# Optimization experiments

Measured on AMD Instinct MI355X. Metric: run time of the kernel, lower is better.

Reference implementation:

```python
import jax, jax.numpy as jnp
import numpy as np

D_MODEL = 1536
NUM_HEADS = 16
QUERY_GROUPS = 4
HEAD_DIM = D_MODEL // NUM_HEADS  # 96
HEADS_PER_GROUP = NUM_HEADS // QUERY_GROUPS
THETA = 10000.0


def _grid_positions(grid_t, grid_h, grid_w):
    # [N, 3] lookup table of (t, h, w) coords, N = T*H*W, 'ij' meshgrid order
    t, h, w = jnp.meshgrid(jnp.arange(grid_t), jnp.arange(grid_h), jnp.arange(grid_w), indexing='ij')
    return jnp.stack([t.reshape(-1), h.reshape(-1), w.reshape(-1)], axis=-1)


def _rope3d(x, positions):
    # x: [B, N, H, head_dim]; rotate three contiguous head_dim//3 slices, one per axis
    B, N, H, hd = x.shape
    dpa = hd // 3            # dims per axis
    P = dpa // 2             # rotation pairs per axis
    freqs = 1.0 / (THETA ** (jnp.arange(P, dtype=jnp.float32) * 2.0 / dpa))  # same for t/h/w
    parts = []
    for axis in range(3):
        ang = positions[:, axis].astype(jnp.float32)[:, None] * freqs[None, :]  # [N, P]
        cos = jnp.cos(ang)[None, :, None, :]  # [1, N, 1, P]
        sin = jnp.sin(ang)[None, :, None, :]
        sl = x[..., axis * dpa:(axis + 1) * dpa].reshape(B, N, H, P, 2)
        x0, x1 = sl[..., 0], sl[..., 1]
        rot = jnp.stack([x0 * cos - x1 * sin, x0 * sin + x1 * cos], axis=-1)
        parts.append(rot.reshape(B, N, H, dpa))
    return jnp.concatenate(parts, axis=-1)


def setup_inputs() -> dict:
    key = jax.random.key(0)
    k1, k2, k3 = jax.random.split(key, 3)
    B, GT, GH, GW = 2, 8, 16, 16
    N = GT * GH * GW  # 2048
    x = jax.random.normal(k1, (B, N, D_MODEL), dtype=jnp.float32)
    qkv_out = NUM_HEADS * HEAD_DIM + 2 * QUERY_GROUPS * HEAD_DIM  # 2304
    w_qkv = jax.random.normal(k2, (qkv_out, D_MODEL), dtype=jnp.float32) * 0.02
    w_o = jax.random.normal(k3, (D_MODEL, D_MODEL), dtype=jnp.float32) * 0.02
    return {"x": x, "w_qkv": w_qkv, "w_o": w_o, "grid_t": GT, "grid_h": GH, "grid_w": GW}


def reference(x, w_qkv, w_o, grid_t, grid_h, grid_w):
    B, N, _ = x.shape
    qkv = x @ w_qkv.T  # [B, N, 2304]
    q_dim = NUM_HEADS * HEAD_DIM
    kv_dim = QUERY_GROUPS * HEAD_DIM
    q = qkv[..., :q_dim].reshape(B, N, NUM_HEADS, HEAD_DIM)
    k = qkv[..., q_dim:q_dim + kv_dim].reshape(B, N, QUERY_GROUPS, HEAD_DIM)
    v = qkv[..., q_dim + kv_dim:].reshape(B, N, QUERY_GROUPS, HEAD_DIM)

    pos = _grid_positions(grid_t, grid_h, grid_w)  # [N, 3]
    q = _rope3d(q, pos)
    k = _rope3d(k, pos)

    # GQA: repeat_interleave kv heads up to num_heads
    k = jnp.repeat(k, HEADS_PER_GROUP, axis=2)
    v = jnp.repeat(v, HEADS_PER_GROUP, axis=2)

    scale = 1.0 / jnp.sqrt(jnp.asarray(HEAD_DIM, dtype=x.dtype))
    scores = jnp.einsum('bnhd,bmhd->bhnm', q, k) * scale
    attn = jax.nn.softmax(scores, axis=-1)
    out = jnp.einsum('bhnm,bmhd->bnhd', attn, v).reshape(B, N, D_MODEL)
    return out @ w_o.T
```

## Files before the change

### kernel.cpp

```cpp
#include <hip/hip_runtime.h>
#include <hip/hip_bf16.h>

typedef short bf16x8 __attribute__((ext_vector_type(8)));
typedef float f32x4  __attribute__((ext_vector_type(4)));

#define NH    16
#define NG    4
#define HD    96
#define DM    1536
#define BB    2
#define NSEQ  2048
#define QKVD  2304
#define MROWS (BB * NSEQ)

__device__ __forceinline__ short bf16_bits(float v)
{
    __hip_bfloat16 h = __float2bfloat16(v);
    return *reinterpret_cast<short*>(&h);
}

__device__ __forceinline__ void stage16(short* dst, const float* src)
{
    float f[16];
    *(float4*)(f + 0)  = *(const float4*)(src + 0);
    *(float4*)(f + 4)  = *(const float4*)(src + 4);
    *(float4*)(f + 8)  = *(const float4*)(src + 8);
    *(float4*)(f + 12) = *(const float4*)(src + 12);
    bf16x8 v0, v1;
    #pragma unroll
    for (int j = 0; j < 8; ++j) { v0[j] = bf16_bits(f[j]); v1[j] = bf16_bits(f[8 + j]); }
    *(bf16x8*)dst = v0;
    *(bf16x8*)(dst + 8) = v1;
}
__device__ __forceinline__ void stage16(short* dst, const __hip_bfloat16* src)
{
    *(bf16x8*)dst       = *(const bf16x8*)src;
    *(bf16x8*)(dst + 8) = *(const bf16x8*)(src + 8);
}

__device__ __forceinline__ void store_c(__hip_bfloat16* p, float v)
{
    *p = __float2bfloat16(v);
}
__device__ __forceinline__ void store_c(float* p, float v) { *p = v; }

__device__ __forceinline__ void gload_lds16(const short* g, short* lds)
{
    __builtin_amdgcn_global_load_lds(
        (const __attribute__((address_space(1))) unsigned int*)g,
        (__attribute__((address_space(3))) unsigned int*)lds,
        16, 0, 0);
}

__global__ __launch_bounds__(256) void cvt3_bf16(
    const float* __restrict__ x,  short* __restrict__ xb,
    const float* __restrict__ wq, short* __restrict__ wqb,
    const float* __restrict__ wo, short* __restrict__ wob)
{
    const int i = blockIdx.x * 256 + threadIdx.x;
    const float* s; short* d; int off;
    if (i < 786432)       { s = x;  d = xb;  off = i; }
    else if (i < 1228800) { s = wq; d = wqb; off = i - 786432; }
    else                  { s = wo; d = wob; off = i - 1228800; }
    float f[8];
    *(float4*)(f + 0) = *(const float4*)(s + (size_t)off * 8);
    *(float4*)(f + 4) = *(const float4*)(s + (size_t)off * 8 + 4);
    bf16x8 v;
    #pragma unroll
    for (int j = 0; j < 8; ++j) v[j] = bf16_bits(f[j]);
    *(bf16x8*)(d + (size_t)off * 8) = v;
}

template <typename TC>
__global__ __launch_bounds__(256) void gemm_async(
    const short* __restrict__ A,
    const short* __restrict__ B,
    TC* __restrict__ C,
    int M, int Nc, int K, int lda, int ldb, int nbx)
{
    __shared__ __align__(16) short As[128][32];
    __shared__ __align__(16) short Bs[128][32];

    const int tid  = threadIdx.x;
    const int wave = tid >> 6;
    const int lane = tid & 63;
    const int quad = lane >> 4;
    const int l16  = lane & 15;
    const int wm = (wave >> 1) * 64;
    const int wn = (wave & 1) * 64;

    const int cpx = gridDim.x >> 3;
    const int swz = (blockIdx.x & 7) * cpx + (blockIdx.x >> 3);
    const int bx  = swz % nbx;
    const int by  = swz / nbx;
    const int m0 = by * 128;
    const int n0 = bx * 128;

    const int lrow = lane >> 2;
    const int lcol = (lane & 3) * 8;

    f32x4 acc[4][4] = {};

    for (int k0 = 0; k0 < K; k0 += 32) {
        __syncthreads();
        #pragma unroll
        for (int i = 0; i < 2; ++i) {
            const int j = wave * 2 + i;
            gload_lds16(A + (size_t)(m0 + j * 16 + lrow) * lda + k0 + lcol, &As[j * 16][0]);
            gload_lds16(B + (size_t)(n0 + j * 16 + lrow) * ldb + k0 + lcol, &Bs[j * 16][0]);
        }
        __syncthreads();

        bf16x8 af[4], bfr[4];
        #pragma unroll
        for (int i = 0; i < 4; ++i)
            af[i] = *(const bf16x8*)&As[wm + i * 16 + l16][quad * 8];
        #pragma unroll
        for (int j = 0; j < 4; ++j)
            bfr[j] = *(const bf16x8*)&Bs[wn + j * 16 + l16][quad * 8];
        #pragma unroll
        for (int i = 0; i < 4; ++i)
            #pragma unroll
            for (int j = 0; j < 4; ++j)
                acc[i][j] = __builtin_amdgcn_mfma_f32_16x16x32_bf16(
                    af[i], bfr[j], acc[i][j], 0, 0, 0);
    }

    #pragma unroll
    for (int i = 0; i < 4; ++i)
      #pragma unroll
      for (int j = 0; j < 4; ++j)
        #pragma unroll
        for (int r = 0; r < 4; ++r) {
            const int row = m0 + wm + i * 16 + quad * 4 + r;
            const int col = n0 + wn + j * 16 + l16;
            store_c(C + (size_t)row * Nc + col, acc[i][j][r]);
        }
}

#define KSTR 40

template <typename TA, typename TB, typename TC>
__global__ __launch_bounds__(256) void gemm_tiled(
    const TA* __restrict__ A,
    const TB* __restrict__ B,
    TC* __restrict__ C,
    int M, int Nc, int K, int lda)
{
    __shared__ __align__(16) short As[128][KSTR];
    __shared__ __align__(16) short Bs[128][KSTR];

    const int tid  = threadIdx.x;
    const int wave = tid >> 6;
    const int lane = tid & 63;
    const int quad = lane >> 4;
    const int l16  = lane & 15;
    const int wm = (wave >> 1) * 64;
    const int wn = (wave & 1) * 64;
    const int m0 = blockIdx.y * 128;
    const int n0 = blockIdx.x * 128;

    const int srow  = tid >> 1;
    const int skseg = (tid & 1) << 4;
    const TA* Asrc = A + (size_t)(m0 + srow) * lda + skseg;
    const TB* Bsrc = B + (size_t)(n0 + srow) * K + skseg;

    f32x4 acc[4][4] = {};

    for (int k0 = 0; k0 < K; k0 += 32) {
        __syncthreads();
        stage16(&As[srow][skseg], Asrc + k0);
        stage16(&Bs[srow][skseg], Bsrc + k0);
        __syncthreads();

        bf16x8 af[4], bfr[4];
        #pragma unroll
        for (int i = 0; i < 4; ++i)
            af[i] = *(const bf16x8*)&As[wm + i * 16 + l16][quad * 8];
        #pragma unroll
        for (int j = 0; j < 4; ++j)
            bfr[j] = *(const bf16x8*)&Bs[wn + j * 16 + l16][quad * 8];
        #pragma unroll
        for (int i = 0; i < 4; ++i)
            #pragma unroll
            for (int j = 0; j < 4; ++j)
                acc[i][j] = __builtin_amdgcn_mfma_f32_16x16x32_bf16(
                    af[i], bfr[j], acc[i][j], 0, 0, 0);
    }

    #pragma unroll
    for (int i = 0; i < 4; ++i)
      #pragma unroll
      for (int j = 0; j < 4; ++j)
        #pragma unroll
        for (int r = 0; r < 4; ++r) {
            const int row = m0 + wm + i * 16 + quad * 4 + r;
            const int col = n0 + wn + j * 16 + l16;
            store_c(C + (size_t)row * Nc + col, acc[i][j][r]);
        }
}

__global__ __launch_bounds__(256) void rope_inplace(__hip_bfloat16* qkv)
{
    const int e = blockIdx.x * 256 + threadIdx.x;
    if (e >= MROWS * 20 * 48) return;
    const int p2   = e % 48;
    const int t2   = e / 48;
    const int slot = t2 % 20;
    const int r    = t2 / 20;
    const int n    = r & (NSEQ - 1);

    const int pt = n >> 8;
    const int ph = (n >> 4) & 15;
    const int pw = n & 15;

    const int axis = p2 >> 4;
    const int lp   = p2 & 15;
    const int d0   = axis * 32 + 2 * lp;
    const int pos  = (axis == 0) ? pt : ((axis == 1) ? ph : pw);

    const int col = (slot < 16) ? (slot * HD + d0)
                                : (DM + (slot - 16) * HD + d0);
    __hip_bfloat16* p = qkv + (size_t)r * QKVD + col;

    const float x0 = __bfloat162float(p[0]);
    const float x1 = __bfloat162float(p[1]);
    const float freq = exp2f(-(float)lp * 0.8304820237f);
    float s, c;
    sincosf((float)pos * freq, &s, &c);
    p[0] = __float2bfloat16(x0 * c - x1 * s);
    p[1] = __float2bfloat16(x0 * s + x1 * c);
}

#define KVSTRIDE 196608

__global__ __launch_bounds__(256) void kv_scatter(
    const __hip_bfloat16* __restrict__ qkv,
    short* __restrict__ Kbuf,
    short* __restrict__ Vtbuf)
{
    const int tid = threadIdx.x;
    const int n0  = blockIdx.x * 64;
    const int bg  = blockIdx.y;
    const int b = bg >> 2, g = bg & 3;
    const size_t qbase = (size_t)(b * NSEQ + n0) * QKVD;

    for (int s = tid; s < 768; s += 256) {
        const int row  = s / 12;
        const int c8   = s - row * 12;
        const int kk   = c8 >> 2;
        const int quad = c8 & 3;
        const int n    = n0 + row;
        bf16x8 v = *(const bf16x8*)(qkv + qbase + (size_t)row * QKVD + DM + g * HD + c8 * 8);
        short* dst = Kbuf + (size_t)bg * KVSTRIDE
                   + ((size_t)((n >> 4) * 3 + kk) << 9)
                   + ((quad << 4) + (n & 15)) * 8;
        *(bf16x8*)dst = v;
    }

    const int row  = tid & 63;
    const int n    = n0 + row;
    const int dseg = (tid >> 6) * 24;
    const int jj   = n & 63;
    const int half = jj >> 5;
    const int quad = (jj >> 3) & 3;
    const int e    = jj & 7;
    const __hip_bfloat16* vsrc =
        qkv + qbase + (size_t)row * QKVD + DM + NG * HD + g * HD + dseg;
    short* vbase = Vtbuf + (size_t)bg * KVSTRIDE + ((size_t)((n >> 6) * 12) << 9);
    #pragma unroll
    for (int u8 = 0; u8 < 3; ++u8) {
        short tmp[8];
        *(bf16x8*)tmp = *(const bf16x8*)(vsrc + u8 * 8);
        #pragma unroll
        for (int u = 0; u < 8; ++u) {
            const int d   = dseg + u8 * 8 + u;
            const int dt  = d >> 4;
            const int l16 = d & 15;
            vbase[(((dt << 1) + half) << 9) + ((quad << 4) + l16) * 8 + e] = tmp[u];
        }
    }
}

#define QT 64
#define KC 64
#define PSTR 72

__global__ __launch_bounds__(256) void flash_attn(
    __hip_bfloat16* __restrict__ qkv,
    const short* __restrict__ Kbuf,
    const short* __restrict__ Vtbuf)
{
    __shared__ __align__(16) short KsLin[6144];
    __shared__ __align__(16) short VtLin[6144];
    __shared__ __align__(16) short Pw[4][16][PSTR];

    const int tid  = threadIdx.x;
    const int wave = tid >> 6;
    const int lane = tid & 63;
    const int quad = lane >> 4;
    const int l16  = lane & 15;

    const int id  = blockIdx.x;
    const int bg  = id & 7;
    const int k   = id >> 3;
    const int b   = bg >> 2, g = bg & 3;
    const int h   = g * 4 + (k & 3);
    const int n0  = (k >> 2) * QT;

    const short* Kc = Kbuf  + (size_t)bg * KVSTRIDE;
    const short* Vc = Vtbuf + (size_t)bg * KVSTRIDE;
    const int lane8 = lane * 8;

    const __hip_bfloat16* Qb = qkv + (size_t)(b * NSEQ + n0 + wave * 16) * QKVD + h * HD;
    bf16x8 qa[3];
    #pragma unroll
    for (int kk = 0; kk < 3; ++kk)
        qa[kk] = *(const bf16x8*)(Qb + (size_t)l16 * QKVD + kk * 32 + quad * 8);

    f32x4 o[6] = {};
    float psum[4] = {0.f, 0.f, 0.f, 0.f};
    const float c1 = 0.14724434f;
    const float c2 = -5.7707802f;
    const int sw = l16 >> 2;

    for (int j0 = 0; j0 < NSEQ; j0 += KC) {
        __syncthreads();
        {
            const short* Kch = Kc + ((size_t)((j0 >> 4) * 3) << 9);
            const short* Vch = Vc + ((size_t)((j0 >> 6) * 12) << 9);
            const short* sb = (wave < 2) ? Kch : Vch;
            short* db       = (wave < 2) ? KsLin : VtLin;
            #pragma unroll
            for (int i = 0; i < 6; ++i) {
                const int t = (wave & 1) * 6 + i;
                gload_lds16(sb + ((size_t)t << 9) + lane8, db + (t << 9));
            }
        }
        __syncthreads();

        f32x4 S[4] = {};
        #pragma unroll
        for (int nt = 0; nt < 4; ++nt) {
            bf16x8 kf[3];
            #pragma unroll
            for (int kk = 0; kk < 3; ++kk)
                kf[kk] = *(const bf16x8*)&KsLin[((nt * 3 + kk) << 9) + lane8];
            #pragma unroll
            for (int kk = 0; kk < 3; ++kk)
                S[nt] = __builtin_amdgcn_mfma_f32_16x16x32_bf16(qa[kk], kf[kk], S[nt], 0, 0, 0);
        }

        #pragma unroll
        for (int nt = 0; nt < 4; ++nt) {
            const int cb   = nt * 2 + (l16 >> 3);
            const int colp = ((cb ^ quad) << 3) + (l16 & 7);
            #pragma unroll
            for (int r = 0; r < 4; ++r) {
                const float p = exp2f(fmaf(S[nt][r], c1, c2));
                psum[r] += p;
                Pw[wave][quad * 4 + r][colp] = bf16_bits(p);
            }
        }

        bf16x8 pa0 = *(const bf16x8*)&Pw[wave][l16][(quad ^ sw) << 3];
        bf16x8 pa1 = *(const bf16x8*)&Pw[wave][l16][((quad ^ sw) + 4) << 3];
        #pragma unroll
        for (int dt = 0; dt < 6; ++dt) {
            bf16x8 vb0 = *(const bf16x8*)&VtLin[((dt * 2 + 0) << 9) + lane8];
            bf16x8 vb1 = *(const bf16x8*)&VtLin[((dt * 2 + 1) << 9) + lane8];
            o[dt] = __builtin_amdgcn_mfma_f32_16x16x32_bf16(pa0, vb0, o[dt], 0, 0, 0);
            o[dt] = __builtin_amdgcn_mfma_f32_16x16x32_bf16(pa1, vb1, o[dt], 0, 0, 0);
        }
    }

    #pragma unroll
    for (int off = 1; off < 16; off <<= 1)
        #pragma unroll
        for (int r = 0; r < 4; ++r)
            psum[r] += __shfl_xor(psum[r], off);
    float inv_l[4];
    #pragma unroll
    for (int r = 0; r < 4; ++r) inv_l[r] = 1.f / psum[r];

    #pragma unroll
    for (int dt = 0; dt < 6; ++dt)
        #pragma unroll
        for (int r = 0; r < 4; ++r) {
            __hip_bfloat16* op =
                qkv + (size_t)(b * NSEQ + n0 + wave * 16 + quad * 4 + r) * QKVD
                    + h * HD + dt * 16 + l16;
            *op = __float2bfloat16(o[dt][r] * inv_l[r]);
        }
}

extern "C" void kernel_launch(void* const* d_in, const int* in_sizes, int n_in,
                              void* d_out, int out_size, void* d_ws, size_t ws_size,
                              hipStream_t stream)
{
    const float* x    = (const float*)d_in[0];
    const float* wqkv = (const float*)d_in[1];
    const float* wo   = (const float*)d_in[2];

    __hip_bfloat16* qkv = (__hip_bfloat16*)d_ws;
    short* xb    = (short*)d_out;
    short* wqb   = (short*)((char*)d_out + 12582912);
    short* Kbuf  = (short*)d_out;
    short* Vtbuf = (short*)((char*)d_out + 3145728);

    const bool wo_in_ws = ws_size >= 23592960;
    short* wob = wo_in_ws ? (short*)((char*)d_ws + 18874368) : (short*)d_out;

    cvt3_bf16<<<wo_in_ws ? 5952 : 4800, 256, 0, stream>>>(x, xb, wqkv, wqb, wo, wob);

    gemm_async<__hip_bfloat16>
        <<<(QKVD / 128) * (MROWS / 128), 256, 0, stream>>>(
            xb, wqb, qkv, MROWS, QKVD, DM, DM, DM, QKVD / 128);

    rope_inplace<<<(MROWS * 20 * 48) / 256, 256, 0, stream>>>(qkv);
    kv_scatter<<<dim3(NSEQ / 64, BB * NG), 256, 0, stream>>>(qkv, Kbuf, Vtbuf);
    flash_attn<<<dim3(NSEQ / QT * BB * NH, 1), 256, 0, stream>>>(qkv, Kbuf, Vtbuf);

    if (wo_in_ws) {
        gemm_async<float>
            <<<(DM / 128) * (MROWS / 128), 256, 0, stream>>>(
                (const short*)qkv, wob, (float*)d_out, MROWS, DM, DM, QKVD, DM, DM / 128);
    } else {
        gemm_tiled<__hip_bfloat16, float, float>
            <<<dim3(DM / 128, MROWS / 128), 256, 0, stream>>>(
                qkv, wo, (float*)d_out, MROWS, DM, DM, QKVD);
    }
}
```

Before: 284.1 us.

## Process two 16-row query tiles per wave in flash attention

Doubles the query tile per block from 64 to 128 rows, so each wave computes two 16-row MFMA tiles against every K/V chunk it stages in LDS. Each K and V fragment read from LDS and each global-to-LDS chunk load now serves twice as many queries, which cuts K/V traffic and synchronisation per unit of work. In exchange, accumulator and register pressure roughly double, which may lower occupancy. There are also half as many blocks to spread across the compute units, and this relies on the launch grid matching the new tile size.

```diff
diff --git a/kernel.cpp b/kernel.cpp
--- a/kernel.cpp
+++ b/kernel.cpp
@@ -282,7 +282,7 @@
     }
 }
 
-#define QT 64
+#define QT 128
 #define KC 64
 #define PSTR 72
 
@@ -293,7 +293,7 @@
 {
     __shared__ __align__(16) short KsLin[6144];
     __shared__ __align__(16) short VtLin[6144];
-    __shared__ __align__(16) short Pw[4][16][PSTR];
+    __shared__ __align__(16) short Pw[4][32][PSTR];
 
     const int tid  = threadIdx.x;
     const int wave = tid >> 6;
@@ -312,14 +312,18 @@
     const short* Vc = Vtbuf + (size_t)bg * KVSTRIDE;
     const int lane8 = lane * 8;
 
-    const __hip_bfloat16* Qb = qkv + (size_t)(b * NSEQ + n0 + wave * 16) * QKVD + h * HD;
-    bf16x8 qa[3];
-    #pragma unroll
-    for (int kk = 0; kk < 3; ++kk)
-        qa[kk] = *(const bf16x8*)(Qb + (size_t)l16 * QKVD + kk * 32 + quad * 8);
-
-    f32x4 o[6] = {};
-    float psum[4] = {0.f, 0.f, 0.f, 0.f};
+    bf16x8 qa[2][3];
+    #pragma unroll
+    for (int mt = 0; mt < 2; ++mt) {
+        const __hip_bfloat16* Qb =
+            qkv + (size_t)(b * NSEQ + n0 + wave * 32 + mt * 16 + l16) * QKVD + h * HD;
+        #pragma unroll
+        for (int kk = 0; kk < 3; ++kk)
+            qa[mt][kk] = *(const bf16x8*)(Qb + kk * 32 + quad * 8);
+    }
+
+    f32x4 o[2][6] = {};
+    float psum[2][4] = {};
     const float c1 = 0.14724434f;
     const float c2 = -5.7707802f;
     const int sw = l16 >> 2;
@@ -339,7 +343,7 @@
         }
         __syncthreads();
 
-        f32x4 S[4] = {};
+        f32x4 S0[4] = {}, S1[4] = {};
         #pragma unroll
         for (int nt = 0; nt < 4; ++nt) {
             bf16x8 kf[3];
@@ -347,8 +351,10 @@
             for (int kk = 0; kk < 3; ++kk)
                 kf[kk] = *(const bf16x8*)&KsLin[((nt * 3 + kk) << 9) + lane8];
             #pragma unroll
-            for (int kk = 0; kk < 3; ++kk)
-                S[nt] = __builtin_amdgcn_mfma_f32_16x16x32_bf16(qa[kk], kf[kk], S[nt], 0, 0, 0);
+            for (int kk = 0; kk < 3; ++kk) {
+                S0[nt] = __builtin_amdgcn_mfma_f32_16x16x32_bf16(qa[0][kk], kf[kk], S0[nt], 0, 0, 0);
+                S1[nt] = __builtin_amdgcn_mfma_f32_16x16x32_bf16(qa[1][kk], kf[kk], S1[nt], 0, 0, 0);
+            }
         }
 
         #pragma unroll
@@ -357,41 +363,57 @@
             const int colp = ((cb ^ quad) << 3) + (l16 & 7);
             #pragma unroll
             for (int r = 0; r < 4; ++r) {
-                const float p = exp2f(fmaf(S[nt][r], c1, c2));
-                psum[r] += p;
-                Pw[wave][quad * 4 + r][colp] = bf16_bits(p);
+                const float p0 = exp2f(fmaf(S0[nt][r], c1, c2));
+                const float p1 = exp2f(fmaf(S1[nt][r], c1, c2));
+                psum[0][r] += p0;
+                psum[1][r] += p1;
+                Pw[wave][quad * 4 + r][colp]      = bf16_bits(p0);
+                Pw[wave][16 + quad * 4 + r][colp] = bf16_bits(p1);
             }
         }
 
-        bf16x8 pa0 = *(const bf16x8*)&Pw[wave][l16][(quad ^ sw) << 3];
-        bf16x8 pa1 = *(const bf16x8*)&Pw[wave][l16][((quad ^ sw) + 4) << 3];
+        bf16x8 pa[2][2];
+        #pragma unroll
+        for (int mt = 0; mt < 2; ++mt) {
+            pa[mt][0] = *(const bf16x8*)&Pw[wave][mt * 16 + l16][(quad ^ sw) << 3];
+            pa[mt][1] = *(const bf16x8*)&Pw[wave][mt * 16 + l16][((quad ^ sw) + 4) << 3];
+        }
         #pragma unroll
         for (int dt = 0; dt < 6; ++dt) {
             bf16x8 vb0 = *(const bf16x8*)&VtLin[((dt * 2 + 0) << 9) + lane8];
             bf16x8 vb1 = *(const bf16x8*)&VtLin[((dt * 2 + 1) << 9) + lane8];
-            o[dt] = __builtin_amdgcn_mfma_f32_16x16x32_bf16(pa0, vb0, o[dt], 0, 0, 0);
-            o[dt] = __builtin_amdgcn_mfma_f32_16x16x32_bf16(pa1, vb1, o[dt], 0, 0, 0);
+            #pragma unroll
+            for (int mt = 0; mt < 2; ++mt) {
+                o[mt][dt] = __builtin_amdgcn_mfma_f32_16x16x32_bf16(pa[mt][0], vb0, o[mt][dt], 0, 0, 0);
+                o[mt][dt] = __builtin_amdgcn_mfma_f32_16x16x32_bf16(pa[mt][1], vb1, o[mt][dt], 0, 0, 0);
+            }
         }
     }
 
     #pragma unroll
     for (int off = 1; off < 16; off <<= 1)
         #pragma unroll
-        for (int r = 0; r < 4; ++r)
-            psum[r] += __shfl_xor(psum[r], off);
-    float inv_l[4];
-    #pragma unroll
-    for (int r = 0; r < 4; ++r) inv_l[r] = 1.f / psum[r];
-
-    #pragma unroll
-    for (int dt = 0; dt < 6; ++dt)
-        #pragma unroll
-        for (int r = 0; r < 4; ++r) {
-            __hip_bfloat16* op =
-                qkv + (size_t)(b * NSEQ + n0 + wave * 16 + quad * 4 + r) * QKVD
-                    + h * HD + dt * 16 + l16;
-            *op = __float2bfloat16(o[dt][r] * inv_l[r]);
-        }
+        for (int mt = 0; mt < 2; ++mt)
+            #pragma unroll
+            for (int r = 0; r < 4; ++r)
+                psum[mt][r] += __shfl_xor(psum[mt][r], off);
+    float inv_l[2][4];
+    #pragma unroll
+    for (int mt = 0; mt < 2; ++mt)
+        #pragma unroll
+        for (int r = 0; r < 4; ++r) inv_l[mt][r] = 1.f / psum[mt][r];
+
+    #pragma unroll
+    for (int mt = 0; mt < 2; ++mt)
+        #pragma unroll
+        for (int dt = 0; dt < 6; ++dt)
+            #pragma unroll
+            for (int r = 0; r < 4; ++r) {
+                __hip_bfloat16* op =
+                    qkv + (size_t)(b * NSEQ + n0 + wave * 32 + mt * 16 + quad * 4 + r) * QKVD
+                        + h * HD + dt * 16 + l16;
+                *op = __float2bfloat16(o[mt][dt][r] * inv_l[mt][r]);
+            }
 }
 
 extern "C" void kernel_launch(void* const* d_in, const int* in_sizes, int n_in,
```

Result: no change. 288.8 us (+1.7%).
